# Performance work log

Measured on AMD Instinct MI355X. Metric: run time of the kernel, lower is better.

Reference implementation:

```python
import jax, jax.numpy as jnp
import numpy as np

MAX_SPAN_WIDTH = 10  # width_embedding has MAX_SPAN_WIDTH+1 rows


def setup_inputs() -> dict:
    key = jax.random.key(0)
    ks = jax.random.split(key, 10)
    B, S, H = 256, 512, 768
    WDIM, NLAB = 25, 42
    CIN = H * 2 + WDIM * 2 + H  # 2354
    seq_out = jax.random.normal(ks[0], (B, S, H), dtype=jnp.float32)
    e1_pos = jax.random.randint(ks[1], (B,), 0, 255)
    e2_pos = jax.random.randint(ks[2], (B,), 0, S)
    e1_word_len = jax.random.randint(ks[3], (B,), 0, 30)
    e2_word_len = jax.random.randint(ks[4], (B,), 0, 30)
    width_emb = jax.random.normal(ks[5], (MAX_SPAN_WIDTH + 1, WDIM), dtype=jnp.float32)
    W1 = jax.random.normal(ks[6], (CIN, H), dtype=jnp.float32) * (1.0 / np.sqrt(CIN))
    b1 = jnp.zeros((H,), dtype=jnp.float32)
    W2 = jax.random.normal(ks[7], (H, NLAB), dtype=jnp.float32) * (1.0 / np.sqrt(H))
    b2 = jnp.zeros((NLAB,), dtype=jnp.float32)
    return {"seq_out": seq_out, "e1_pos": e1_pos, "e2_pos": e2_pos,
            "e1_word_len": e1_word_len, "e2_word_len": e2_word_len,
            "width_emb": width_emb, "W1": W1, "b1": b1, "W2": W2, "b2": b2}


def reference(seq_out, e1_pos, e2_pos, e1_word_len, e2_word_len,
              width_emb, W1, b1, W2, b2):
    B, S, H = seq_out.shape
    batch = jnp.arange(B)
    # gather entity token reps
    e1_repr = seq_out[batch, e1_pos]  # [B,H]
    e2_repr = seq_out[batch, e2_pos]  # [B,H]
    # width embeddings (clamped to max span width)
    e1_w = width_emb[jnp.clip(e1_word_len, 0, MAX_SPAN_WIDTH)]  # [B,Wdim]
    e2_w = width_emb[jnp.clip(e2_word_len, 0, MAX_SPAN_WIDTH)]
    # masked mean over tokens strictly between e1_pos and e2_pos
    pos = jnp.arange(S)
    mask = ((pos[None, :] > e1_pos[:, None]) & (pos[None, :] < e2_pos[:, None])).astype(seq_out.dtype)  # [B,S]
    cnt = mask.sum(axis=-1, keepdims=True)  # [B,1]
    ctx = jnp.einsum('bs,bsh->bh', mask, seq_out) / jnp.maximum(cnt, 1.0)
    ctx = jnp.where(cnt > 0, ctx, jnp.zeros_like(ctx))  # zeros when e2 <= e1+1
    combined = jnp.concatenate([e1_repr, e2_repr, e1_w, e2_w, ctx], axis=-1)  # [B,2354]
    # dropout is identity at inference
    h = jax.nn.relu(combined @ W1 + b1)
    logits = h @ W2 + b2
    return logits
```

## Files before the change

kernel.cpp:

```cpp
#include <hip/hip_runtime.h>

#define BATCH 256
#define SEQ   512
#define HDIM  768
#define WDIM  25
#define NLAB  42
#define CIN   2354
#define CINP  2432
#define E1W_OFF 1536
#define E2W_OFF 1561
#define CTX_OFF 1586
#define MAXW  10
#define NCHUNK 4

__global__ __launch_bounds__(192) void span_partial(
    const float* __restrict__ seq,
    const int* __restrict__ e1p, const int* __restrict__ e2p,
    float* __restrict__ comb, float* __restrict__ ctxpart) {
  const int b = blockIdx.y;
  const int cidx = blockIdx.x;
  const int t = threadIdx.x;
  const int e1 = e1p[b];
  const int e2 = e2p[b];
  const float4* row4 = (const float4*)(seq + (size_t)b * SEQ * HDIM);

  if (cidx == 0) {
    float4* crow4 = (float4*)(comb + (size_t)b * CINP);
    crow4[t]       = row4[e1 * 192 + t];
    crow4[192 + t] = row4[e2 * 192 + t];
  }

  const int s0 = e1 + 1;
  const int n = max(e2 - s0, 0);
  const int clen = (n + NCHUNK - 1) / NCHUNK;
  const int t0 = s0 + cidx * clen;
  const int t1 = min(t0 + clen, e2);

  float4 acc = make_float4(0.f, 0.f, 0.f, 0.f);
  const float4* p = row4 + (size_t)t0 * 192 + t;
  int tok = t0;
  for (; tok + 4 <= t1; tok += 4) {
    float4 v0 = p[0], v1 = p[192], v2 = p[384], v3 = p[576];
    acc.x += (v0.x + v1.x) + (v2.x + v3.x);
    acc.y += (v0.y + v1.y) + (v2.y + v3.y);
    acc.z += (v0.z + v1.z) + (v2.z + v3.z);
    acc.w += (v0.w + v1.w) + (v2.w + v3.w);
    p += 768;
  }
  for (; tok < t1; ++tok) {
    float4 v = *p;
    acc.x += v.x; acc.y += v.y; acc.z += v.z; acc.w += v.w;
    p += 192;
  }
  float4* cp = (float4*)ctxpart;
  cp[((size_t)cidx * BATCH + b) * (HDIM / 4) + t] = acc;
}

__global__ __launch_bounds__(192) void combine(
    const int* __restrict__ e1p, const int* __restrict__ e2p,
    const int* __restrict__ e1l, const int* __restrict__ e2l,
    const float* __restrict__ wemb,
    const float* __restrict__ ctxpart,
    float* __restrict__ comb) {
  const int b = blockIdx.x;
  const int t = threadIdx.x;
  const int n = max(e2p[b] - e1p[b] - 1, 0);
  const float inv = (n > 0) ? 1.f / (float)n : 0.f;
  float* crow = comb + (size_t)b * CINP;

  const float4* cp = (const float4*)ctxpart;
  const size_t base = (size_t)b * (HDIM / 4) + t;
  const size_t str = (size_t)BATCH * (HDIM / 4);
  float4 a0 = cp[base];
  float4 a1 = cp[base + str];
  float4 a2 = cp[base + 2 * str];
  float4 a3 = cp[base + 3 * str];
  crow[CTX_OFF + 4 * t + 0] = ((a0.x + a1.x) + (a2.x + a3.x)) * inv;
  crow[CTX_OFF + 4 * t + 1] = ((a0.y + a1.y) + (a2.y + a3.y)) * inv;
  crow[CTX_OFF + 4 * t + 2] = ((a0.z + a1.z) + (a2.z + a3.z)) * inv;
  crow[CTX_OFF + 4 * t + 3] = ((a0.w + a1.w) + (a2.w + a3.w)) * inv;

  if (t < WDIM) {
    int w = e1l[b]; w = w < 0 ? 0 : (w > MAXW ? MAXW : w);
    crow[E1W_OFF + t] = wemb[w * WDIM + t];
  } else if (t >= 64 && t < 64 + WDIM) {
    int tt = t - 64;
    int w = e2l[b]; w = w < 0 ? 0 : (w > MAXW ? MAXW : w);
    crow[E2W_OFF + tt] = wemb[w * WDIM + tt];
  }
  if (t < CINP - CIN) crow[CIN + t] = 0.f;
}

#define BM 32
#define BN 64
#define BK 32
#define SPLITK 4
#define KCH 608
#define ASTR 34
#define BSTR 68

__global__ __launch_bounds__(256) void gemm1(
    const float* __restrict__ comb,
    const float* __restrict__ W1,
    float* __restrict__ hpart) {
  const int nt = blockIdx.x;
  const int mt = blockIdx.y;
  const int ks = blockIdx.z;
  const int tid = threadIdx.x;
  const int k0 = ks * KCH;
  const int m0 = mt * BM;
  const int n0 = nt * BN;

  __shared__ float As[2][BK * ASTR];
  __shared__ float Bs[2][BK * BSTR];

  const int am = tid >> 3;
  const int ak = (tid & 7) * 4;
  const int bk = tid >> 4;
  const int bn = (tid & 15) * 4;
  const int tx = tid & 15;
  const int ty = tid >> 4;

  const float* Aptr = comb + (size_t)(m0 + am) * CINP + k0 + ak;
  const float* Bptr = W1 + (size_t)(k0 + bk) * HDIM + n0 + bn;

  const float4 z4 = make_float4(0.f, 0.f, 0.f, 0.f);
  float4 ar, br0, br1;

  ar = *(const float4*)Aptr;
  br0 = (k0 + bk < CIN) ? *(const float4*)Bptr : z4;
  br1 = (k0 + bk + 16 < CIN) ? *(const float4*)(Bptr + 16 * HDIM) : z4;
  As[0][(ak + 0) * ASTR + am] = ar.x;
  As[0][(ak + 1) * ASTR + am] = ar.y;
  As[0][(ak + 2) * ASTR + am] = ar.z;
  As[0][(ak + 3) * ASTR + am] = ar.w;
  *(float4*)&Bs[0][bk * BSTR + bn] = br0;
  *(float4*)&Bs[0][(bk + 16) * BSTR + bn] = br1;
  __syncthreads();

  float acc[2][4] = {{0.f,0.f,0.f,0.f},{0.f,0.f,0.f,0.f}};
  const int NT = KCH / BK;
  int cur = 0;
  for (int t = 0; t < NT; ++t) {
    if (t + 1 < NT) {
      const float* Ap = Aptr + (t + 1) * BK;
      const float* Bp = Bptr + (size_t)(t + 1) * BK * HDIM;
      int kg = k0 + (t + 1) * BK + bk;
      ar = *(const float4*)Ap;
      br0 = (kg < CIN) ? *(const float4*)Bp : z4;
      br1 = (kg + 16 < CIN) ? *(const float4*)(Bp + 16 * HDIM) : z4;
    }
    const float* Asc = As[cur];
    const float* Bsc = Bs[cur];
#pragma unroll
    for (int k = 0; k < BK; ++k) {
      float a0 = Asc[k * ASTR + 2 * ty];
      float a1 = Asc[k * ASTR + 2 * ty + 1];
      float4 bv = *(const float4*)&Bsc[k * BSTR + tx * 4];
      acc[0][0] += a0 * bv.x; acc[0][1] += a0 * bv.y;
      acc[0][2] += a0 * bv.z; acc[0][3] += a0 * bv.w;
      acc[1][0] += a1 * bv.x; acc[1][1] += a1 * bv.y;
      acc[1][2] += a1 * bv.z; acc[1][3] += a1 * bv.w;
    }
    if (t + 1 < NT) {
      __syncthreads();
      int nxt = cur ^ 1;
      As[nxt][(ak + 0) * ASTR + am] = ar.x;
      As[nxt][(ak + 1) * ASTR + am] = ar.y;
      As[nxt][(ak + 2) * ASTR + am] = ar.z;
      As[nxt][(ak + 3) * ASTR + am] = ar.w;
      *(float4*)&Bs[nxt][bk * BSTR + bn] = br0;
      *(float4*)&Bs[nxt][(bk + 16) * BSTR + bn] = br1;
      __syncthreads();
      cur = nxt;
    }
  }

  float* outp = hpart + (size_t)ks * BATCH * HDIM;
#pragma unroll
  for (int i = 0; i < 2; ++i) {
    int m = m0 + 2 * ty + i;
    float4 v = make_float4(acc[i][0], acc[i][1], acc[i][2], acc[i][3]);
    *(float4*)&outp[(size_t)m * HDIM + n0 + tx * 4] = v;
  }
}

__global__ __launch_bounds__(256) void gemm2(
    const float* __restrict__ hpart,
    const float* __restrict__ b1,
    const float* __restrict__ W2,
    const float* __restrict__ b2,
    float* __restrict__ out) {
  const int m = blockIdx.x;
  const int tid = threadIdx.x;
  __shared__ float hs[HDIM];
  __shared__ float part[6 * NLAB];

  const float* p = hpart + (size_t)m * HDIM;
  const size_t str = (size_t)BATCH * HDIM;
  for (int i = tid; i < HDIM; i += 256) {
    float v = (p[i] + p[i + str]) + (p[i + 2 * str] + p[i + 3 * str]) + b1[i];
    hs[i] = v > 0.f ? v : 0.f;
  }
  __syncthreads();

  if (tid < 252) {
    const int g = tid / NLAB;
    const int c = tid - g * NLAB;
    const int kk0 = g * 128;
    float a = 0.f;
#pragma unroll 8
    for (int j = 0; j < 128; ++j) {
      int k = kk0 + j;
      a += hs[k] * W2[k * NLAB + c];
    }
    part[g * NLAB + c] = a;
  }
  __syncthreads();

  if (tid < NLAB) {
    float r = b2[tid];
#pragma unroll
    for (int g = 0; g < 6; ++g) r += part[g * NLAB + tid];
    out[m * NLAB + tid] = r;
  }
}

extern "C" void kernel_launch(void* const* d_in, const int* in_sizes, int n_in,
                              void* d_out, int out_size, void* d_ws, size_t ws_size,
                              hipStream_t stream) {
  const float* seq  = (const float*)d_in[0];
  const int*   e1p  = (const int*)d_in[1];
  const int*   e2p  = (const int*)d_in[2];
  const int*   e1l  = (const int*)d_in[3];
  const int*   e2l  = (const int*)d_in[4];
  const float* wemb = (const float*)d_in[5];
  const float* W1   = (const float*)d_in[6];
  const float* b1   = (const float*)d_in[7];
  const float* W2   = (const float*)d_in[8];
  const float* b2   = (const float*)d_in[9];
  float* out = (float*)d_out;

  float* comb    = (float*)d_ws;
  float* ctxpart = comb + (size_t)BATCH * CINP;
  float* hpart   = ctxpart + (size_t)NCHUNK * BATCH * HDIM;

  span_partial<<<dim3(NCHUNK, BATCH), 192, 0, stream>>>(seq, e1p, e2p, comb, ctxpart);
  combine<<<BATCH, 192, 0, stream>>>(e1p, e2p, e1l, e2l, wemb, ctxpart, comb);
  gemm1<<<dim3(HDIM / BN, BATCH / BM, SPLITK), 256, 0, stream>>>(comb, W1, hpart);
  gemm2<<<BATCH, 256, 0, stream>>>(hpart, b1, W2, b2, out);
}
```

Before: 527.7 us.

## Fuse span-combine into GEMM1 A-loads and double span-sum chunks

Removes the separate combine kernel and the materialized combined-feature matrix. GEMM1 now builds its A tile on the fly from the entity rows in seq, the width embeddings, and the partial context sums, which it reduces and scales inline. The span reduction is split into 8 chunks instead of 4 to expose more parallelism, using a padded per-row layout so the context sums line up for float4 loads. The cost moves into GEMM1: each tile re-reduces 8 partials and takes branchy, partly scalar loads, and this work is repeated for every N-tile.

Measured after the change: 541.7 us. 2.6% more time.

```diff
diff --git a/kernel.cpp b/kernel.cpp
--- a/kernel.cpp
+++ b/kernel.cpp
@@ -11,24 +11,19 @@
 #define E2W_OFF 1561
 #define CTX_OFF 1586
 #define MAXW  10
-#define NCHUNK 4
+#define NCHUNK 8
+#define CPW   776
 
 __global__ __launch_bounds__(192) void span_partial(
     const float* __restrict__ seq,
     const int* __restrict__ e1p, const int* __restrict__ e2p,
-    float* __restrict__ comb, float* __restrict__ ctxpart) {
+    float* __restrict__ ctxpart) {
   const int b = blockIdx.y;
   const int cidx = blockIdx.x;
   const int t = threadIdx.x;
   const int e1 = e1p[b];
   const int e2 = e2p[b];
   const float4* row4 = (const float4*)(seq + (size_t)b * SEQ * HDIM);
-
-  if (cidx == 0) {
-    float4* crow4 = (float4*)(comb + (size_t)b * CINP);
-    crow4[t]       = row4[e1 * 192 + t];
-    crow4[192 + t] = row4[e2 * 192 + t];
-  }
 
   const int s0 = e1 + 1;
   const int n = max(e2 - s0, 0);
@@ -52,43 +47,49 @@
     acc.x += v.x; acc.y += v.y; acc.z += v.z; acc.w += v.w;
     p += 192;
   }
-  float4* cp = (float4*)ctxpart;
-  cp[((size_t)cidx * BATCH + b) * (HDIM / 4) + t] = acc;
-}
-
-__global__ __launch_bounds__(192) void combine(
-    const int* __restrict__ e1p, const int* __restrict__ e2p,
-    const int* __restrict__ e1l, const int* __restrict__ e2l,
-    const float* __restrict__ wemb,
-    const float* __restrict__ ctxpart,
-    float* __restrict__ comb) {
-  const int b = blockIdx.x;
-  const int t = threadIdx.x;
-  const int n = max(e2p[b] - e1p[b] - 1, 0);
-  const float inv = (n > 0) ? 1.f / (float)n : 0.f;
-  float* crow = comb + (size_t)b * CINP;
-
-  const float4* cp = (const float4*)ctxpart;
-  const size_t base = (size_t)b * (HDIM / 4) + t;
-  const size_t str = (size_t)BATCH * (HDIM / 4);
-  float4 a0 = cp[base];
-  float4 a1 = cp[base + str];
-  float4 a2 = cp[base + 2 * str];
-  float4 a3 = cp[base + 3 * str];
-  crow[CTX_OFF + 4 * t + 0] = ((a0.x + a1.x) + (a2.x + a3.x)) * inv;
-  crow[CTX_OFF + 4 * t + 1] = ((a0.y + a1.y) + (a2.y + a3.y)) * inv;
-  crow[CTX_OFF + 4 * t + 2] = ((a0.z + a1.z) + (a2.z + a3.z)) * inv;
-  crow[CTX_OFF + 4 * t + 3] = ((a0.w + a1.w) + (a2.w + a3.w)) * inv;
-
-  if (t < WDIM) {
-    int w = e1l[b]; w = w < 0 ? 0 : (w > MAXW ? MAXW : w);
-    crow[E1W_OFF + t] = wemb[w * WDIM + t];
-  } else if (t >= 64 && t < 64 + WDIM) {
-    int tt = t - 64;
-    int w = e2l[b]; w = w < 0 ? 0 : (w > MAXW ? MAXW : w);
-    crow[E2W_OFF + tt] = wemb[w * WDIM + tt];
-  }
-  if (t < CINP - CIN) crow[CIN + t] = 0.f;
+  float* dst = ctxpart + ((size_t)cidx * BATCH + b) * CPW + 2 + 4 * t;
+  *(float2*)(dst)     = make_float2(acc.x, acc.y);
+  *(float2*)(dst + 2) = make_float2(acc.z, acc.w);
+}
+
+__device__ __forceinline__ float a_elem(int k,
+    const float* __restrict__ re1, const float* __restrict__ re2,
+    const float* __restrict__ we1, const float* __restrict__ we2,
+    const float* __restrict__ cpm, float inv) {
+  if (k < HDIM)     return re1[k];
+  if (k < 2*HDIM)   return re2[k - HDIM];
+  if (k < E2W_OFF)  return we1[k - E1W_OFF];
+  if (k < CTX_OFF)  return we2[k - E2W_OFF];
+  if (k < CIN) {
+    const int off = 2 + (k - CTX_OFF);
+    float s = 0.f;
+#pragma unroll
+    for (int c = 0; c < NCHUNK; ++c) s += cpm[(size_t)c * BATCH * CPW + off];
+    return s * inv;
+  }
+  return 0.f;
+}
+
+__device__ __forceinline__ float4 a_vec(int k,
+    const float* __restrict__ re1, const float* __restrict__ re2,
+    const float* __restrict__ we1, const float* __restrict__ we2,
+    const float* __restrict__ cpm, float inv) {
+  if (k + 3 < HDIM) return *(const float4*)(re1 + k);
+  if (k >= HDIM && k + 3 < 2*HDIM) return *(const float4*)(re2 + (k - HDIM));
+  if (k >= CTX_OFF + 2 && k + 3 < CIN) {
+    const int off = 2 + (k - CTX_OFF);
+    float sx = 0.f, sy = 0.f, sz = 0.f, sw = 0.f;
+#pragma unroll
+    for (int c = 0; c < NCHUNK; ++c) {
+      float4 v = *(const float4*)(cpm + (size_t)c * BATCH * CPW + off);
+      sx += v.x; sy += v.y; sz += v.z; sw += v.w;
+    }
+    return make_float4(sx * inv, sy * inv, sz * inv, sw * inv);
+  }
+  return make_float4(a_elem(k,     re1, re2, we1, we2, cpm, inv),
+                     a_elem(k + 1, re1, re2, we1, we2, cpm, inv),
+                     a_elem(k + 2, re1, re2, we1, we2, cpm, inv),
+                     a_elem(k + 3, re1, re2, we1, we2, cpm, inv));
 }
 
 #define BM 32
@@ -100,7 +101,11 @@
 #define BSTR 68
 
 __global__ __launch_bounds__(256) void gemm1(
-    const float* __restrict__ comb,
+    const float* __restrict__ seq,
+    const int* __restrict__ e1p, const int* __restrict__ e2p,
+    const int* __restrict__ e1l, const int* __restrict__ e2l,
+    const float* __restrict__ wemb,
+    const float* __restrict__ ctxpart,
     const float* __restrict__ W1,
     float* __restrict__ hpart) {
   const int nt = blockIdx.x;
@@ -121,13 +126,24 @@
   const int tx = tid & 15;
   const int ty = tid >> 4;
 
-  const float* Aptr = comb + (size_t)(m0 + am) * CINP + k0 + ak;
+  const int m = m0 + am;
+  const int e1 = e1p[m];
+  const int e2 = e2p[m];
+  int w1i = e1l[m]; w1i = w1i < 0 ? 0 : (w1i > MAXW ? MAXW : w1i);
+  int w2i = e2l[m]; w2i = w2i < 0 ? 0 : (w2i > MAXW ? MAXW : w2i);
+  const float* re1 = seq + ((size_t)m * SEQ + e1) * HDIM;
+  const float* re2 = seq + ((size_t)m * SEQ + e2) * HDIM;
+  const float* we1 = wemb + w1i * WDIM;
+  const float* we2 = wemb + w2i * WDIM;
+  const float* cpm = ctxpart + (size_t)m * CPW;
+  const int nspan = max(e2 - e1 - 1, 0);
+  const float inv = nspan > 0 ? 1.f / (float)nspan : 0.f;
+
   const float* Bptr = W1 + (size_t)(k0 + bk) * HDIM + n0 + bn;
-
   const float4 z4 = make_float4(0.f, 0.f, 0.f, 0.f);
   float4 ar, br0, br1;
 
-  ar = *(const float4*)Aptr;
+  ar  = a_vec(k0 + ak, re1, re2, we1, we2, cpm, inv);
   br0 = (k0 + bk < CIN) ? *(const float4*)Bptr : z4;
   br1 = (k0 + bk + 16 < CIN) ? *(const float4*)(Bptr + 16 * HDIM) : z4;
   As[0][(ak + 0) * ASTR + am] = ar.x;
@@ -143,12 +159,11 @@
   int cur = 0;
   for (int t = 0; t < NT; ++t) {
     if (t + 1 < NT) {
-      const float* Ap = Aptr + (t + 1) * BK;
+      const int kn = k0 + (t + 1) * BK;
       const float* Bp = Bptr + (size_t)(t + 1) * BK * HDIM;
-      int kg = k0 + (t + 1) * BK + bk;
-      ar = *(const float4*)Ap;
-      br0 = (kg < CIN) ? *(const float4*)Bp : z4;
-      br1 = (kg + 16 < CIN) ? *(const float4*)(Bp + 16 * HDIM) : z4;
+      ar  = a_vec(kn + ak, re1, re2, we1, we2, cpm, inv);
+      br0 = (kn + bk < CIN) ? *(const float4*)Bp : z4;
+      br1 = (kn + bk + 16 < CIN) ? *(const float4*)(Bp + 16 * HDIM) : z4;
     }
     const float* Asc = As[cur];
     const float* Bsc = Bs[cur];
@@ -179,9 +194,9 @@
   float* outp = hpart + (size_t)ks * BATCH * HDIM;
 #pragma unroll
   for (int i = 0; i < 2; ++i) {
-    int m = m0 + 2 * ty + i;
+    int mr = m0 + 2 * ty + i;
     float4 v = make_float4(acc[i][0], acc[i][1], acc[i][2], acc[i][3]);
-    *(float4*)&outp[(size_t)m * HDIM + n0 + tx * 4] = v;
+    *(float4*)&outp[(size_t)mr * HDIM + n0 + tx * 4] = v;
   }
 }
 
@@ -241,12 +256,11 @@
   const float* b2   = (const float*)d_in[9];
   float* out = (float*)d_out;
 
-  float* comb    = (float*)d_ws;
-  float* ctxpart = comb + (size_t)BATCH * CINP;
-  float* hpart   = ctxpart + (size_t)NCHUNK * BATCH * HDIM;
-
-  span_partial<<<dim3(NCHUNK, BATCH), 192, 0, stream>>>(seq, e1p, e2p, comb, ctxpart);
-  combine<<<BATCH, 192, 0, stream>>>(e1p, e2p, e1l, e2l, wemb, ctxpart, comb);
-  gemm1<<<dim3(HDIM / BN, BATCH / BM, SPLITK), 256, 0, stream>>>(comb, W1, hpart);
+  float* ctxpart = (float*)d_ws;
+  float* hpart   = ctxpart + (size_t)NCHUNK * BATCH * CPW;
+
+  span_partial<<<dim3(NCHUNK, BATCH), 192, 0, stream>>>(seq, e1p, e2p, ctxpart);
+  gemm1<<<dim3(HDIM / BN, BATCH / BM, SPLITK), 256, 0, stream>>>(
+      seq, e1p, e2p, e1l, e2l, wemb, ctxpart, W1, hpart);
   gemm2<<<BATCH, 256, 0, stream>>>(hpart, b1, W2, b2, out);
 }
```

## Use 4x4 register tiles in gemm1, double split-K and span chunks

Applied to the files above, without the earlier changes.

The first GEMM now computes a 64x64 output tile per block with a 4x4 register micro-tile and a K step of 16, which raises arithmetic intensity per shared-memory load. Split-K goes from 4 to 8 so the grid stays large enough to fill the GPU despite the bigger tiles. The span-sum kernel splits each span into 8 chunks instead of 4 for more parallelism. The cost is more partial-sum traffic in the reduction kernels, and the workspace grows because there are twice as many partial buffers.

Result: no change. 525.5 us (-0.4%).

```diff
diff --git a/kernel.cpp b/kernel.cpp
--- a/kernel.cpp
+++ b/kernel.cpp
@@ -11,7 +11,7 @@
 #define E2W_OFF 1561
 #define CTX_OFF 1586
 #define MAXW  10
-#define NCHUNK 4
+#define NCHUNK 8
 
 __global__ __launch_bounds__(192) void span_partial(
     const float* __restrict__ seq,
@@ -71,14 +71,16 @@
   const float4* cp = (const float4*)ctxpart;
   const size_t base = (size_t)b * (HDIM / 4) + t;
   const size_t str = (size_t)BATCH * (HDIM / 4);
-  float4 a0 = cp[base];
-  float4 a1 = cp[base + str];
-  float4 a2 = cp[base + 2 * str];
-  float4 a3 = cp[base + 3 * str];
-  crow[CTX_OFF + 4 * t + 0] = ((a0.x + a1.x) + (a2.x + a3.x)) * inv;
-  crow[CTX_OFF + 4 * t + 1] = ((a0.y + a1.y) + (a2.y + a3.y)) * inv;
-  crow[CTX_OFF + 4 * t + 2] = ((a0.z + a1.z) + (a2.z + a3.z)) * inv;
-  crow[CTX_OFF + 4 * t + 3] = ((a0.w + a1.w) + (a2.w + a3.w)) * inv;
+  float sx = 0.f, sy = 0.f, sz = 0.f, sw = 0.f;
+#pragma unroll
+  for (int c = 0; c < NCHUNK; ++c) {
+    float4 v = cp[base + (size_t)c * str];
+    sx += v.x; sy += v.y; sz += v.z; sw += v.w;
+  }
+  crow[CTX_OFF + 4 * t + 0] = sx * inv;
+  crow[CTX_OFF + 4 * t + 1] = sy * inv;
+  crow[CTX_OFF + 4 * t + 2] = sz * inv;
+  crow[CTX_OFF + 4 * t + 3] = sw * inv;
 
   if (t < WDIM) {
     int w = e1l[b]; w = w < 0 ? 0 : (w > MAXW ? MAXW : w);
@@ -91,12 +93,12 @@
   if (t < CINP - CIN) crow[CIN + t] = 0.f;
 }
 
-#define BM 32
+#define BM 64
 #define BN 64
-#define BK 32
-#define SPLITK 4
-#define KCH 608
-#define ASTR 34
+#define BK 16
+#define SPLITK 8
+#define KCH 304
+#define ASTR 68
 #define BSTR 68
 
 __global__ __launch_bounds__(256) void gemm1(
@@ -114,8 +116,8 @@
   __shared__ float As[2][BK * ASTR];
   __shared__ float Bs[2][BK * BSTR];
 
-  const int am = tid >> 3;
-  const int ak = (tid & 7) * 4;
+  const int am = tid >> 2;
+  const int ak = (tid & 3) * 4;
   const int bk = tid >> 4;
   const int bn = (tid & 15) * 4;
   const int tx = tid & 15;
@@ -123,44 +125,46 @@
 
   const float* Aptr = comb + (size_t)(m0 + am) * CINP + k0 + ak;
   const float* Bptr = W1 + (size_t)(k0 + bk) * HDIM + n0 + bn;
-
   const float4 z4 = make_float4(0.f, 0.f, 0.f, 0.f);
-  float4 ar, br0, br1;
+  float4 ar, br;
 
   ar = *(const float4*)Aptr;
-  br0 = (k0 + bk < CIN) ? *(const float4*)Bptr : z4;
-  br1 = (k0 + bk + 16 < CIN) ? *(const float4*)(Bptr + 16 * HDIM) : z4;
+  br = (k0 + bk < CIN) ? *(const float4*)Bptr : z4;
   As[0][(ak + 0) * ASTR + am] = ar.x;
   As[0][(ak + 1) * ASTR + am] = ar.y;
   As[0][(ak + 2) * ASTR + am] = ar.z;
   As[0][(ak + 3) * ASTR + am] = ar.w;
-  *(float4*)&Bs[0][bk * BSTR + bn] = br0;
-  *(float4*)&Bs[0][(bk + 16) * BSTR + bn] = br1;
+  *(float4*)&Bs[0][bk * BSTR + bn] = br;
   __syncthreads();
 
-  float acc[2][4] = {{0.f,0.f,0.f,0.f},{0.f,0.f,0.f,0.f}};
+  float acc[4][4];
+#pragma unroll
+  for (int i = 0; i < 4; ++i)
+#pragma unroll
+    for (int j = 0; j < 4; ++j) acc[i][j] = 0.f;
+
   const int NT = KCH / BK;
   int cur = 0;
   for (int t = 0; t < NT; ++t) {
     if (t + 1 < NT) {
-      const float* Ap = Aptr + (t + 1) * BK;
-      const float* Bp = Bptr + (size_t)(t + 1) * BK * HDIM;
-      int kg = k0 + (t + 1) * BK + bk;
-      ar = *(const float4*)Ap;
-      br0 = (kg < CIN) ? *(const float4*)Bp : z4;
-      br1 = (kg + 16 < CIN) ? *(const float4*)(Bp + 16 * HDIM) : z4;
+      ar = *(const float4*)(Aptr + (t + 1) * BK);
+      br = (k0 + (t + 1) * BK + bk < CIN)
+               ? *(const float4*)(Bptr + (size_t)(t + 1) * BK * HDIM) : z4;
     }
     const float* Asc = As[cur];
     const float* Bsc = Bs[cur];
 #pragma unroll
     for (int k = 0; k < BK; ++k) {
-      float a0 = Asc[k * ASTR + 2 * ty];
-      float a1 = Asc[k * ASTR + 2 * ty + 1];
-      float4 bv = *(const float4*)&Bsc[k * BSTR + tx * 4];
-      acc[0][0] += a0 * bv.x; acc[0][1] += a0 * bv.y;
-      acc[0][2] += a0 * bv.z; acc[0][3] += a0 * bv.w;
-      acc[1][0] += a1 * bv.x; acc[1][1] += a1 * bv.y;
-      acc[1][2] += a1 * bv.z; acc[1][3] += a1 * bv.w;
+      float4 av = *(const float4*)&Asc[k * ASTR + 4 * ty];
+      float4 bv = *(const float4*)&Bsc[k * BSTR + 4 * tx];
+      acc[0][0] += av.x * bv.x; acc[0][1] += av.x * bv.y;
+      acc[0][2] += av.x * bv.z; acc[0][3] += av.x * bv.w;
+      acc[1][0] += av.y * bv.x; acc[1][1] += av.y * bv.y;
+      acc[1][2] += av.y * bv.z; acc[1][3] += av.y * bv.w;
+      acc[2][0] += av.z * bv.x; acc[2][1] += av.z * bv.y;
+      acc[2][2] += av.z * bv.z; acc[2][3] += av.z * bv.w;
+      acc[3][0] += av.w * bv.x; acc[3][1] += av.w * bv.y;
+      acc[3][2] += av.w * bv.z; acc[3][3] += av.w * bv.w;
     }
     if (t + 1 < NT) {
       __syncthreads();
@@ -169,8 +173,7 @@
       As[nxt][(ak + 1) * ASTR + am] = ar.y;
       As[nxt][(ak + 2) * ASTR + am] = ar.z;
       As[nxt][(ak + 3) * ASTR + am] = ar.w;
-      *(float4*)&Bs[nxt][bk * BSTR + bn] = br0;
-      *(float4*)&Bs[nxt][(bk + 16) * BSTR + bn] = br1;
+      *(float4*)&Bs[nxt][bk * BSTR + bn] = br;
       __syncthreads();
       cur = nxt;
     }
@@ -178,10 +181,10 @@
 
   float* outp = hpart + (size_t)ks * BATCH * HDIM;
 #pragma unroll
-  for (int i = 0; i < 2; ++i) {
-    int m = m0 + 2 * ty + i;
+  for (int i = 0; i < 4; ++i) {
+    int mr = m0 + 4 * ty + i;
     float4 v = make_float4(acc[i][0], acc[i][1], acc[i][2], acc[i][3]);
-    *(float4*)&outp[(size_t)m * HDIM + n0 + tx * 4] = v;
+    *(float4*)&outp[(size_t)mr * HDIM + n0 + 4 * tx] = v;
   }
 }
 
@@ -199,7 +202,9 @@
   const float* p = hpart + (size_t)m * HDIM;
   const size_t str = (size_t)BATCH * HDIM;
   for (int i = tid; i < HDIM; i += 256) {
-    float v = (p[i] + p[i + str]) + (p[i + 2 * str] + p[i + 3 * str]) + b1[i];
+    float v = b1[i];
+#pragma unroll
+    for (int g = 0; g < SPLITK; ++g) v += p[i + g * str];
     hs[i] = v > 0.f ? v : 0.f;
   }
   __syncthreads();
```
